# Optimization experiments

Hardware: AMD Instinct MI355X
Metric: run time of the kernel (lower is better)

Reference implementation:

```python
import jax, jax.numpy as jnp
import numpy as np

B, T, C, H = 2, 2048, 1024, 16
SCALE = 0.02

def setup_inputs() -> dict:
    key = jax.random.key(0)
    ks = jax.random.split(key, 6)
    x = jax.random.normal(ks[0], (B, T, C), dtype=jnp.float32)
    Wq = jax.random.normal(ks[1], (C, C), dtype=jnp.float32) * SCALE
    Wk = jax.random.normal(ks[2], (C, C), dtype=jnp.float32) * SCALE
    Wv = jax.random.normal(ks[3], (C, C), dtype=jnp.float32) * SCALE
    Wp = jax.random.normal(ks[4], (C, C), dtype=jnp.float32) * SCALE
    z = jnp.zeros((C,), dtype=jnp.float32)
    return {"x": x, "Wq": Wq, "bq": z, "Wk": Wk, "bk": z, "Wv": Wv, "bv": z, "Wp": Wp, "bp": z}

def reference(x, Wq, bq, Wk, bk, Wv, bv, Wp, bp):
    b, t, c = x.shape
    hd = c // H  # head dim
    def split_heads(y):
        return y.reshape(b, t, H, hd).transpose(0, 2, 1, 3)  # [b,h,t,hd]
    q = split_heads(x @ Wq + bq)
    k = split_heads(x @ Wk + bk)
    v = split_heads(x @ Wv + bv)
    # explicit [b,h,t,t] scores with causal mask (tril), scaled by 1/sqrt(hd)
    att = jnp.einsum('bhqd,bhkd->bhqk', q, k) * (1.0 / jnp.sqrt(jnp.asarray(hd, x.dtype)))
    causal = jnp.tril(jnp.ones((t, t), dtype=bool))
    att = jnp.where(causal[None, None], att, jnp.asarray(-jnp.inf, att.dtype))
    att = jax.nn.softmax(att, axis=-1)
    y = jnp.einsum('bhqk,bhkd->bhqd', att, v)  # [b,h,t,hd]
    y = y.transpose(0, 2, 1, 3).reshape(b, t, c)
    return y @ Wp + bp
```

## Files before the change

kernel.cpp:

```cpp
#include <hip/hip_runtime.h>

typedef unsigned short u16;
typedef short s16x8 __attribute__((ext_vector_type(8)));
typedef unsigned short u16x4 __attribute__((ext_vector_type(4)));
typedef float f32x4 __attribute__((ext_vector_type(4)));

#define Bdim 2
#define Tdim 2048
#define Cdim 1024
#define Hn   16
#define HD   64
#define Mdim (Bdim*Tdim)

static __device__ __forceinline__ u16 f2b(float f) {
  union { float f; unsigned u; } x; x.f = f;
  unsigned r = (x.u + 0x7fffu + ((x.u >> 16) & 1u)) >> 16;
  return (u16)r;
}

static __device__ __forceinline__ void gload_lds16(const void* g, void* l) {
  __builtin_amdgcn_global_load_lds((const __attribute__((address_space(1))) void*)g,
                                   (__attribute__((address_space(3))) void*)l, 16, 0, 0);
}

__global__ __launch_bounds__(256) void cast_x_kernel(const float* __restrict__ in,
                                                     u16* __restrict__ out) {
  int i = (blockIdx.x * 256 + threadIdx.x) * 4;
  float4 f = *reinterpret_cast<const float4*>(in + i);
  uint2 o;
  o.x = (unsigned)f2b(f.x) | ((unsigned)f2b(f.y) << 16);
  o.y = (unsigned)f2b(f.z) | ((unsigned)f2b(f.w) << 16);
  *reinterpret_cast<uint2*>(out + i) = o;
}

__global__ __launch_bounds__(256) void transW_kernel(const float* __restrict__ Wq,
                                                     const float* __restrict__ Wk,
                                                     const float* __restrict__ Wv,
                                                     const float* __restrict__ Wp,
                                                     u16* __restrict__ Wt3,
                                                     u16* __restrict__ Wpt) {
  __shared__ float tile[32][33];
  const int z = blockIdx.z;
  const float* W = (z == 0) ? Wq : (z == 1) ? Wk : (z == 2) ? Wv : Wp;
  u16* dst = (z < 3) ? (Wt3 + (size_t)z * Cdim * Cdim) : Wpt;
  const int k0 = blockIdx.y * 32, n0 = blockIdx.x * 32;
  const int tx = threadIdx.x & 31, ty = threadIdx.x >> 5;
#pragma unroll
  for (int i = 0; i < 4; ++i)
    tile[ty + i * 8][tx] = W[(size_t)(k0 + ty + i * 8) * Cdim + n0 + tx];
  __syncthreads();
#pragma unroll
  for (int i = 0; i < 4; ++i)
    dst[(size_t)(n0 + ty + i * 8) * Cdim + k0 + tx] = f2b(tile[tx][ty + i * 8]);
}

template <int MODE>
__global__ __launch_bounds__(256) void gemm_bf16(
    const u16* __restrict__ A, const u16* __restrict__ Bt,
    const float* __restrict__ b0, const float* __restrict__ b1,
    const float* __restrict__ b2,
    u16* __restrict__ q_out, u16* __restrict__ k_out, u16* __restrict__ v_out,
    float* __restrict__ c_out) {
  __shared__ __attribute__((aligned(16))) u16 As[128 * 32];
  __shared__ __attribute__((aligned(16))) u16 Bs[128 * 32];
  const int tid = threadIdx.x;
  const int lane = tid & 63, wave = tid >> 6;
  const int m0 = blockIdx.y * 128, n0 = blockIdx.x * 128;
  const int wm = (wave >> 1) * 64, wn = (wave & 1) * 64;
  const int lr = lane & 15, lk = (lane >> 4) * 8;
  const int srow = lane >> 2, scol = (lane & 3) * 8;
  f32x4 acc[4][4] = {};
  for (int k0 = 0; k0 < Cdim; k0 += 32) {
    __syncthreads();
#pragma unroll
    for (int i = 0; i < 2; ++i) {
      const int slot = wave * 2 + i;
      const int row = slot * 16 + srow;
      gload_lds16(&A[(size_t)(m0 + row) * Cdim + k0 + scol], (char*)As + slot * 1024);
      gload_lds16(&Bt[(size_t)(n0 + row) * Cdim + k0 + scol], (char*)Bs + slot * 1024);
    }
    __syncthreads();
    s16x8 af[4], bf[4];
#pragma unroll
    for (int i = 0; i < 4; ++i) {
      af[i] = *reinterpret_cast<const s16x8*>(&As[(wm + i * 16 + lr) * 32 + lk]);
      bf[i] = *reinterpret_cast<const s16x8*>(&Bs[(wn + i * 16 + lr) * 32 + lk]);
    }
#pragma unroll
    for (int mi = 0; mi < 4; ++mi)
#pragma unroll
      for (int ni = 0; ni < 4; ++ni)
        acc[mi][ni] = __builtin_amdgcn_mfma_f32_16x16x32_bf16(af[mi], bf[ni], acc[mi][ni], 0, 0, 0);
  }
  const int lc = lane & 15, lr4 = (lane >> 4) * 4;
  if (MODE == 0) {
    const int seg = n0 >> 10;
    const float* bias = (seg == 0) ? b0 : (seg == 1) ? b1 : b2;
    const int nb = n0 & 1023;
    if (seg < 2) {
      u16* dst = (seg == 0) ? q_out : k_out;
#pragma unroll
      for (int mi = 0; mi < 4; ++mi)
#pragma unroll
        for (int ni = 0; ni < 4; ++ni)
#pragma unroll
          for (int j = 0; j < 4; ++j) {
            int m = m0 + wm + mi * 16 + lr4 + j;
            int n = nb + wn + ni * 16 + lc;
            float v = acc[mi][ni][j] + bias[n];
            int b = m >> 11, t = m & 2047, h = n >> 6, d = n & 63;
            dst[(((size_t)(b * Hn + h)) * Tdim + t) * HD + d] = f2b(v);
          }
    } else {
#pragma unroll
      for (int mi = 0; mi < 4; ++mi)
#pragma unroll
        for (int ni = 0; ni < 4; ++ni) {
          int mbase = m0 + wm + mi * 16 + lr4;
          int n = nb + wn + ni * 16 + lc;
          float bn = bias[n];
          u16x4 w;
#pragma unroll
          for (int j = 0; j < 4; ++j) w[j] = f2b(acc[mi][ni][j] + bn);
          int b = mbase >> 11, t = mbase & 2047, h = n >> 6, d = n & 63;
          *reinterpret_cast<u16x4*>(
              &v_out[(((size_t)(b * Hn + h)) * HD + d) * Tdim + t]) = w;
        }
    }
  } else {
#pragma unroll
    for (int mi = 0; mi < 4; ++mi)
#pragma unroll
      for (int ni = 0; ni < 4; ++ni)
#pragma unroll
        for (int j = 0; j < 4; ++j) {
          int m = m0 + wm + mi * 16 + lr4 + j;
          int n = n0 + wn + ni * 16 + lc;
          c_out[(size_t)m * Cdim + n] = acc[mi][ni][j] + b0[n];
        }
  }
}

__global__ __launch_bounds__(256) void attn_kernel(const u16* __restrict__ Qh,
                                                   const u16* __restrict__ Kh,
                                                   const u16* __restrict__ Vt,
                                                   u16* __restrict__ Yb) {
  __shared__ __attribute__((aligned(16))) u16 Ks[2][64 * 64];
  __shared__ __attribute__((aligned(16))) u16 Vs[2][64 * 64];
  __shared__ __attribute__((aligned(16))) u16 Ps[4][16 * 64];
  const int id = blockIdx.x;
  const int bh = id & 31;
  const int qblk = 31 - (id >> 5);
  const int tid = threadIdx.x;
  const int wave = tid >> 6, lane = tid & 63;
  const int lr = lane & 15, lg = lane >> 4;
  const int r0 = qblk * 64 + wave * 16;
  const int q_idx = r0 + lr;
  const u16* Qb = Qh + (size_t)bh * Tdim * HD;
  const u16* Kb = Kh + (size_t)bh * Tdim * HD;
  const u16* Vb = Vt + (size_t)bh * HD * Tdim;
  const float SC = 0.18033688011112042f;

  const int c1 = tid + 256;
  const int kr0 = tid >> 3, kc0 = (tid & 7) * 8, kw0 = kr0 * 64 + (kc0 ^ ((kr0 & 7) * 8));
  const int kr1 = c1 >> 3, kc1 = (c1 & 7) * 8, kw1 = kr1 * 64 + (kc1 ^ ((kr1 & 7) * 8));

  s16x8 bQ[2];
#pragma unroll
  for (int ks = 0; ks < 2; ++ks)
    bQ[ks] = *reinterpret_cast<const s16x8*>(&Qb[(size_t)q_idx * HD + ks * 32 + lg * 8]);

  float m = -1e30f, l = 0.f;
  f32x4 o[4];
#pragma unroll
  for (int di = 0; di < 4; ++di) o[di] = (f32x4){0.f, 0.f, 0.f, 0.f};

  s16x8 kg0, kg1, vg0, vg1;
  {
    kg0 = *reinterpret_cast<const s16x8*>(&Kb[(size_t)kr0 * HD + kc0]);
    kg1 = *reinterpret_cast<const s16x8*>(&Kb[(size_t)kr1 * HD + kc1]);
    vg0 = *reinterpret_cast<const s16x8*>(&Vb[(size_t)kr0 * Tdim + kc0]);
    vg1 = *reinterpret_cast<const s16x8*>(&Vb[(size_t)kr1 * Tdim + kc1]);
    *reinterpret_cast<s16x8*>(&Ks[0][kw0]) = kg0;
    *reinterpret_cast<s16x8*>(&Ks[0][kw1]) = kg1;
    *reinterpret_cast<s16x8*>(&Vs[0][kw0]) = vg0;
    *reinterpret_cast<s16x8*>(&Vs[0][kw1]) = vg1;
  }
  __syncthreads();

  const int swl = (lr & 7) * 8;
  for (int kb = 0; kb <= qblk; ++kb) {
    const int cur = kb & 1;
    if (kb < qblk) {
      const int kn = (kb + 1) * 64;
      kg0 = *reinterpret_cast<const s16x8*>(&Kb[(size_t)(kn + kr0) * HD + kc0]);
      kg1 = *reinterpret_cast<const s16x8*>(&Kb[(size_t)(kn + kr1) * HD + kc1]);
      vg0 = *reinterpret_cast<const s16x8*>(&Vb[(size_t)kr0 * Tdim + kn + kc0]);
      vg1 = *reinterpret_cast<const s16x8*>(&Vb[(size_t)kr1 * Tdim + kn + kc1]);
    }
    const int k0 = kb * 64;
    f32x4 st[4] = {};
#pragma unroll
    for (int ni = 0; ni < 4; ++ni)
#pragma unroll
      for (int ks = 0; ks < 2; ++ks) {
        s16x8 aK = *reinterpret_cast<const s16x8*>(
            &Ks[cur][(ni * 16 + lr) * 64 + ((ks * 32 + lg * 8) ^ swl)]);
        st[ni] = __builtin_amdgcn_mfma_f32_16x16x32_bf16(aK, bQ[ks], st[ni], 0, 0, 0);
      }
#pragma unroll
    for (int ni = 0; ni < 4; ++ni)
#pragma unroll
      for (int j = 0; j < 4; ++j) st[ni][j] *= SC;
    if (kb == qblk) {
#pragma unroll
      for (int ni = 0; ni < 4; ++ni)
#pragma unroll
        for (int j = 0; j < 4; ++j)
          if (k0 + ni * 16 + lg * 4 + j > q_idx) st[ni][j] = -1e30f;
    }
    float t4[4];
#pragma unroll
    for (int ni = 0; ni < 4; ++ni)
      t4[ni] = fmaxf(fmaxf(st[ni][0], st[ni][1]), fmaxf(st[ni][2], st[ni][3]));
    float tm = fmaxf(fmaxf(t4[0], t4[1]), fmaxf(t4[2], t4[3]));
    tm = fmaxf(tm, __shfl_xor(tm, 16));
    tm = fmaxf(tm, __shfl_xor(tm, 32));
    const float mn = fmaxf(m, tm);
    const float corr = exp2f(m - mn);
    m = mn;
    float rs = 0.f;
#pragma unroll
    for (int ni = 0; ni < 4; ++ni) {
      float p0 = exp2f(st[ni][0] - mn), p1 = exp2f(st[ni][1] - mn);
      float p2 = exp2f(st[ni][2] - mn), p3 = exp2f(st[ni][3] - mn);
      st[ni][0] = p0; st[ni][1] = p1; st[ni][2] = p2; st[ni][3] = p3;
      rs += (p0 + p1) + (p2 + p3);
    }
    rs += __shfl_xor(rs, 16);
    rs += __shfl_xor(rs, 32);
    l = l * corr + rs;
#pragma unroll
    for (int di = 0; di < 4; ++di)
#pragma unroll
      for (int j = 0; j < 4; ++j) o[di][j] *= corr;
#pragma unroll
    for (int ni = 0; ni < 4; ++ni) {
      uint2 pw;
      pw.x = (unsigned)f2b(st[ni][0]) | ((unsigned)f2b(st[ni][1]) << 16);
      pw.y = (unsigned)f2b(st[ni][2]) | ((unsigned)f2b(st[ni][3]) << 16);
      *reinterpret_cast<uint2*>(&Ps[wave][lr * 64 + ((ni * 16 + lg * 4) ^ swl)]) = pw;
    }
    s16x8 bP[2];
#pragma unroll
    for (int ks = 0; ks < 2; ++ks)
      bP[ks] = *reinterpret_cast<const s16x8*>(
          &Ps[wave][lr * 64 + ((ks * 32 + lg * 8) ^ swl)]);
#pragma unroll
    for (int di = 0; di < 4; ++di)
#pragma unroll
      for (int ks = 0; ks < 2; ++ks) {
        s16x8 aV = *reinterpret_cast<const s16x8*>(
            &Vs[cur][(di * 16 + lr) * 64 + ((ks * 32 + lg * 8) ^ swl)]);
        o[di] = __builtin_amdgcn_mfma_f32_16x16x32_bf16(aV, bP[ks], o[di], 0, 0, 0);
      }
    __syncthreads();
    if (kb < qblk) {
      const int nxt = cur ^ 1;
      *reinterpret_cast<s16x8*>(&Ks[nxt][kw0]) = kg0;
      *reinterpret_cast<s16x8*>(&Ks[nxt][kw1]) = kg1;
      *reinterpret_cast<s16x8*>(&Vs[nxt][kw0]) = vg0;
      *reinterpret_cast<s16x8*>(&Vs[nxt][kw1]) = vg1;
    }
    __syncthreads();
  }
  const int b = bh >> 4, h = bh & 15;
  const float rl = 1.0f / l;
#pragma unroll
  for (int di = 0; di < 4; ++di) {
    u16x4 w;
#pragma unroll
    for (int j = 0; j < 4; ++j) w[j] = f2b(o[di][j] * rl);
    *reinterpret_cast<u16x4*>(
        &Yb[((size_t)(b * Tdim + q_idx)) * Cdim + h * 64 + di * 16 + lg * 4]) = w;
  }
}

extern "C" void kernel_launch(void* const* d_in, const int* in_sizes, int n_in,
                              void* d_out, int out_size, void* d_ws, size_t ws_size,
                              hipStream_t stream) {
  const float* x  = (const float*)d_in[0];
  const float* Wq = (const float*)d_in[1];
  const float* bq = (const float*)d_in[2];
  const float* Wk = (const float*)d_in[3];
  const float* bk = (const float*)d_in[4];
  const float* Wv = (const float*)d_in[5];
  const float* bv = (const float*)d_in[6];
  const float* Wp = (const float*)d_in[7];
  const float* bp = (const float*)d_in[8];
  float* out = (float*)d_out;
  char* ws = (char*)d_ws;

  u16* xb  = (u16*)(ws);
  u16* Wt3 = (u16*)(ws + ((size_t)8  << 20));
  u16* Wpt = (u16*)(ws + ((size_t)14 << 20));
  u16* Qh  = (u16*)(ws + ((size_t)16 << 20));
  u16* Kh  = (u16*)(ws + ((size_t)24 << 20));
  u16* Vt  = (u16*)(ws + ((size_t)32 << 20));
  u16* Yb  = (u16*)(ws + ((size_t)48 << 20));

  cast_x_kernel<<<4096, 256, 0, stream>>>(x, xb);
  transW_kernel<<<dim3(32, 32, 4), 256, 0, stream>>>(Wq, Wk, Wv, Wp, Wt3, Wpt);
  gemm_bf16<0><<<dim3(24, 32), 256, 0, stream>>>(xb, Wt3, bq, bk, bv, Qh, Kh, Vt, nullptr);
  attn_kernel<<<1024, 256, 0, stream>>>(Qh, Kh, Vt, Yb);
  gemm_bf16<1><<<dim3(8, 32), 256, 0, stream>>>(Yb, Wpt, bp, nullptr, nullptr,
                                                nullptr, nullptr, nullptr, out);
}
```

Before: 214.8 us.

## Use packed bf16 conversion, lazy softmax rescale, MFMA priority, wider weight transpose

Replaces the software bf16 rounding with the hardware v_cvt_pk_bf16_f32 instruction in every kernel. In attention, the score scaling is folded into an fma inside exp2, and the running max with its O/l rescale is skipped unless some lane's new max exceeds the old one by more than 8 (lazy rescale). s_setprio is raised around the MFMA blocks. The weight transpose kernel moves to 64x64 bf16 tiles with vectorised loads and stores. The lazy rescale lets exp values reach up to 2^8 before renormalisation, which carries some precision and overflow risk.

```diff
diff --git a/kernel.cpp b/kernel.cpp
--- a/kernel.cpp
+++ b/kernel.cpp
@@ -18,6 +18,12 @@
   return (u16)r;
 }
 
+static __device__ __forceinline__ unsigned cvt_pk(float lo, float hi) {
+  unsigned r;
+  asm("v_cvt_pk_bf16_f32 %0, %1, %2" : "=v"(r) : "v"(lo), "v"(hi));
+  return r;
+}
+
 static __device__ __forceinline__ void gload_lds16(const void* g, void* l) {
   __builtin_amdgcn_global_load_lds((const __attribute__((address_space(1))) void*)g,
                                    (__attribute__((address_space(3))) void*)l, 16, 0, 0);
@@ -28,8 +34,8 @@
   int i = (blockIdx.x * 256 + threadIdx.x) * 4;
   float4 f = *reinterpret_cast<const float4*>(in + i);
   uint2 o;
-  o.x = (unsigned)f2b(f.x) | ((unsigned)f2b(f.y) << 16);
-  o.y = (unsigned)f2b(f.z) | ((unsigned)f2b(f.w) << 16);
+  o.x = cvt_pk(f.x, f.y);
+  o.y = cvt_pk(f.z, f.w);
   *reinterpret_cast<uint2*>(out + i) = o;
 }
 
@@ -39,19 +45,30 @@
                                                      const float* __restrict__ Wp,
                                                      u16* __restrict__ Wt3,
                                                      u16* __restrict__ Wpt) {
-  __shared__ float tile[32][33];
+  __shared__ u16 tile[64][72];
   const int z = blockIdx.z;
   const float* W = (z == 0) ? Wq : (z == 1) ? Wk : (z == 2) ? Wv : Wp;
   u16* dst = (z < 3) ? (Wt3 + (size_t)z * Cdim * Cdim) : Wpt;
-  const int k0 = blockIdx.y * 32, n0 = blockIdx.x * 32;
-  const int tx = threadIdx.x & 31, ty = threadIdx.x >> 5;
-#pragma unroll
-  for (int i = 0; i < 4; ++i)
-    tile[ty + i * 8][tx] = W[(size_t)(k0 + ty + i * 8) * Cdim + n0 + tx];
+  const int k0 = blockIdx.y * 64, n0 = blockIdx.x * 64;
+  const int tx = threadIdx.x & 15, ty = threadIdx.x >> 4;
+#pragma unroll
+  for (int p = 0; p < 4; ++p) {
+    float4 f = *reinterpret_cast<const float4*>(
+        &W[(size_t)(k0 + ty + p * 16) * Cdim + n0 + tx * 4]);
+    uint2 o;
+    o.x = cvt_pk(f.x, f.y);
+    o.y = cvt_pk(f.z, f.w);
+    *reinterpret_cast<uint2*>(&tile[ty + p * 16][tx * 4]) = o;
+  }
   __syncthreads();
 #pragma unroll
-  for (int i = 0; i < 4; ++i)
-    dst[(size_t)(n0 + ty + i * 8) * Cdim + k0 + tx] = f2b(tile[tx][ty + i * 8]);
+  for (int p = 0; p < 4; ++p) {
+    const int r = ty + p * 16;
+    u16x4 w;
+#pragma unroll
+    for (int jj = 0; jj < 4; ++jj) w[jj] = tile[tx * 4 + jj][r];
+    *reinterpret_cast<u16x4*>(&dst[(size_t)(n0 + r) * Cdim + k0 + tx * 4]) = w;
+  }
 }
 
 template <int MODE>
@@ -102,15 +119,19 @@
 #pragma unroll
       for (int mi = 0; mi < 4; ++mi)
 #pragma unroll
-        for (int ni = 0; ni < 4; ++ni)
-#pragma unroll
-          for (int j = 0; j < 4; ++j) {
-            int m = m0 + wm + mi * 16 + lr4 + j;
-            int n = nb + wn + ni * 16 + lc;
-            float v = acc[mi][ni][j] + bias[n];
-            int b = m >> 11, t = m & 2047, h = n >> 6, d = n & 63;
-            dst[(((size_t)(b * Hn + h)) * Tdim + t) * HD + d] = f2b(v);
-          }
+        for (int ni = 0; ni < 4; ++ni) {
+          int mb = m0 + wm + mi * 16 + lr4;
+          int n = nb + wn + ni * 16 + lc;
+          float bn = bias[n];
+          unsigned p01 = cvt_pk(acc[mi][ni][0] + bn, acc[mi][ni][1] + bn);
+          unsigned p23 = cvt_pk(acc[mi][ni][2] + bn, acc[mi][ni][3] + bn);
+          int b = mb >> 11, t = mb & 2047, h = n >> 6, d = n & 63;
+          size_t base = (((size_t)(b * Hn + h)) * Tdim + t) * HD + d;
+          dst[base]       = (u16)p01;
+          dst[base + 64]  = (u16)(p01 >> 16);
+          dst[base + 128] = (u16)p23;
+          dst[base + 192] = (u16)(p23 >> 16);
+        }
     } else {
 #pragma unroll
       for (int mi = 0; mi < 4; ++mi)
@@ -119,11 +140,11 @@
           int mbase = m0 + wm + mi * 16 + lr4;
           int n = nb + wn + ni * 16 + lc;
           float bn = bias[n];
-          u16x4 w;
-#pragma unroll
-          for (int j = 0; j < 4; ++j) w[j] = f2b(acc[mi][ni][j] + bn);
+          uint2 w;
+          w.x = cvt_pk(acc[mi][ni][0] + bn, acc[mi][ni][1] + bn);
+          w.y = cvt_pk(acc[mi][ni][2] + bn, acc[mi][ni][3] + bn);
           int b = mbase >> 11, t = mbase & 2047, h = n >> 6, d = n & 63;
-          *reinterpret_cast<u16x4*>(
+          *reinterpret_cast<uint2*>(
               &v_out[(((size_t)(b * Hn + h)) * HD + d) * Tdim + t]) = w;
         }
     }
@@ -200,6 +221,7 @@
     }
     const int k0 = kb * 64;
     f32x4 st[4] = {};
+    __builtin_amdgcn_s_setprio(1);
 #pragma unroll
     for (int ni = 0; ni < 4; ++ni)
 #pragma unroll
@@ -208,10 +230,7 @@
             &Ks[cur][(ni * 16 + lr) * 64 + ((ks * 32 + lg * 8) ^ swl)]);
         st[ni] = __builtin_amdgcn_mfma_f32_16x16x32_bf16(aK, bQ[ks], st[ni], 0, 0, 0);
       }
-#pragma unroll
-    for (int ni = 0; ni < 4; ++ni)
-#pragma unroll
-      for (int j = 0; j < 4; ++j) st[ni][j] *= SC;
+    __builtin_amdgcn_s_setprio(0);
     if (kb == qblk) {
 #pragma unroll
       for (int ni = 0; ni < 4; ++ni)
@@ -226,29 +245,35 @@
     float tm = fmaxf(fmaxf(t4[0], t4[1]), fmaxf(t4[2], t4[3]));
     tm = fmaxf(tm, __shfl_xor(tm, 16));
     tm = fmaxf(tm, __shfl_xor(tm, 32));
-    const float mn = fmaxf(m, tm);
-    const float corr = exp2f(m - mn);
-    m = mn;
+    const float tms = tm * SC;
+    if (!__all(tms <= m + 8.0f)) {
+      const float mn = fmaxf(m, tms);
+      const float corr = exp2f(m - mn);
+      l *= corr;
+#pragma unroll
+      for (int di = 0; di < 4; ++di)
+#pragma unroll
+        for (int j = 0; j < 4; ++j) o[di][j] *= corr;
+      m = mn;
+    }
     float rs = 0.f;
 #pragma unroll
     for (int ni = 0; ni < 4; ++ni) {
-      float p0 = exp2f(st[ni][0] - mn), p1 = exp2f(st[ni][1] - mn);
-      float p2 = exp2f(st[ni][2] - mn), p3 = exp2f(st[ni][3] - mn);
+      float p0 = exp2f(fmaf(st[ni][0], SC, -m));
+      float p1 = exp2f(fmaf(st[ni][1], SC, -m));
+      float p2 = exp2f(fmaf(st[ni][2], SC, -m));
+      float p3 = exp2f(fmaf(st[ni][3], SC, -m));
       st[ni][0] = p0; st[ni][1] = p1; st[ni][2] = p2; st[ni][3] = p3;
       rs += (p0 + p1) + (p2 + p3);
     }
     rs += __shfl_xor(rs, 16);
     rs += __shfl_xor(rs, 32);
-    l = l * corr + rs;
-#pragma unroll
-    for (int di = 0; di < 4; ++di)
-#pragma unroll
-      for (int j = 0; j < 4; ++j) o[di][j] *= corr;
+    l += rs;
 #pragma unroll
     for (int ni = 0; ni < 4; ++ni) {
       uint2 pw;
-      pw.x = (unsigned)f2b(st[ni][0]) | ((unsigned)f2b(st[ni][1]) << 16);
-      pw.y = (unsigned)f2b(st[ni][2]) | ((unsigned)f2b(st[ni][3]) << 16);
+      pw.x = cvt_pk(st[ni][0], st[ni][1]);
+      pw.y = cvt_pk(st[ni][2], st[ni][3]);
       *reinterpret_cast<uint2*>(&Ps[wave][lr * 64 + ((ni * 16 + lg * 4) ^ swl)]) = pw;
     }
     s16x8 bP[2];
@@ -256,6 +281,7 @@
     for (int ks = 0; ks < 2; ++ks)
       bP[ks] = *reinterpret_cast<const s16x8*>(
           &Ps[wave][lr * 64 + ((ks * 32 + lg * 8) ^ swl)]);
+    __builtin_amdgcn_s_setprio(1);
 #pragma unroll
     for (int di = 0; di < 4; ++di)
 #pragma unroll
@@ -264,6 +290,7 @@
             &Vs[cur][(di * 16 + lr) * 64 + ((ks * 32 + lg * 8) ^ swl)]);
         o[di] = __builtin_amdgcn_mfma_f32_16x16x32_bf16(aV, bP[ks], o[di], 0, 0, 0);
       }
+    __builtin_amdgcn_s_setprio(0);
     __syncthreads();
     if (kb < qblk) {
       const int nxt = cur ^ 1;
@@ -278,10 +305,10 @@
   const float rl = 1.0f / l;
 #pragma unroll
   for (int di = 0; di < 4; ++di) {
-    u16x4 w;
-#pragma unroll
-    for (int j = 0; j < 4; ++j) w[j] = f2b(o[di][j] * rl);
-    *reinterpret_cast<u16x4*>(
+    uint2 w;
+    w.x = cvt_pk(o[di][0] * rl, o[di][1] * rl);
+    w.y = cvt_pk(o[di][2] * rl, o[di][3] * rl);
+    *reinterpret_cast<uint2*>(
         &Yb[((size_t)(b * Tdim + q_idx)) * Cdim + h * 64 + di * 16 + lg * 4]) = w;
   }
 }
@@ -310,7 +337,7 @@
   u16* Yb  = (u16*)(ws + ((size_t)48 << 20));
 
   cast_x_kernel<<<4096, 256, 0, stream>>>(x, xb);
-  transW_kernel<<<dim3(32, 32, 4), 256, 0, stream>>>(Wq, Wk, Wv, Wp, Wt3, Wpt);
+  transW_kernel<<<dim3(16, 16, 4), 256, 0, stream>>>(Wq, Wk, Wv, Wp, Wt3, Wpt);
   gemm_bf16<0><<<dim3(24, 32), 256, 0, stream>>>(xb, Wt3, bq, bk, bv, Qh, Kh, Vt, nullptr);
   attn_kernel<<<1024, 256, 0, stream>>>(Qh, Kh, Vt, Yb);
   gemm_bf16<1><<<dim3(8, 32), 256, 0, stream>>>(Yb, Wpt, bp, nullptr, nullptr,
```

New measurement: 209.4 us. -2.5%, faster.
